# Performance work log

Measured on AMD Instinct MI355X. Metric: run time of the kernel, lower is better.

The kernel has to match this reference:

```python
import jax, jax.numpy as jnp
import numpy as np

B, C, Hf, Wf, HM, P = 64, 2048, 16, 16, 256, 10  # P = num_parts, NP = graph nodes
NP = P - 1
EPS = 1e-5  # BatchNorm eps

def bn_eval(x, g, b, rm, rv):
    return (x - rm) * jax.lax.rsqrt(rv + EPS) * g + b

def setup_inputs() -> dict:
    key = jax.random.key(0)
    ks = jax.random.split(key, 6)
    return {
        "x_global": jax.random.normal(ks[0], (B, C, Hf, Wf), jnp.float32),
        "x_gcn": jax.random.normal(ks[1], (B, C, Hf, Wf), jnp.float32),
        "mask": jax.random.randint(ks[2], (B, 1, HM, HM), 0, P, jnp.int32),
        "adj": jax.random.uniform(ks[3], (B, NP, NP), jnp.float32),
        "W1": jax.random.normal(ks[4], (C, C), jnp.float32) * 0.02,
        "b1": jnp.zeros((C,), jnp.float32),
        "g1": jnp.ones((NP * C,), jnp.float32), "be1": jnp.zeros((NP * C,), jnp.float32),
        "rm1": jnp.zeros((NP * C,), jnp.float32), "rv1": jnp.ones((NP * C,), jnp.float32),
        "W2": jax.random.normal(ks[5], (C, C), jnp.float32) * 0.02,
        "b2": jnp.zeros((C,), jnp.float32),
        "g2": jnp.ones((NP * C,), jnp.float32), "be2": jnp.zeros((NP * C,), jnp.float32),
        "rm2": jnp.zeros((NP * C,), jnp.float32), "rv2": jnp.ones((NP * C,), jnp.float32),
        "gb_g": jnp.ones((C,), jnp.float32), "gb_b": jnp.zeros((C,), jnp.float32),
        "gb_rm": jnp.zeros((C,), jnp.float32), "gb_rv": jnp.ones((C,), jnp.float32),
        "gn_g": jnp.ones((C,), jnp.float32), "gn_b": jnp.zeros((C,), jnp.float32),
        "gn_rm": jnp.zeros((C,), jnp.float32), "gn_rv": jnp.ones((C,), jnp.float32),
    }

def gc_layer(x, adj, Wt, bias, g, be, rm, rv):
    # GraphConvolution: matmul -> bmm(adj) -> bias -> BN over flattened (B, NP*C)
    s = jnp.einsum('bpc,cd->bpd', x, Wt)
    o = jnp.einsum('bpq,bqd->bpd', adj, s) + bias
    flat = o.reshape(o.shape[0], -1)
    return bn_eval(flat, g, be, rm, rv).reshape(o.shape)

def reference(x_global, x_gcn, mask, adj, W1, b1, g1, be1, rm1, rv1,
              W2, b2, g2, be2, rm2, rv2, gb_g, gb_b, gb_rm, gb_rv,
              gn_g, gn_b, gn_rm, gn_rv):
    # --- global branch: GAP + bottleneck BN (eval) ---
    feat_global = x_global.mean(axis=(2, 3))                      # (B, C)
    bnfeat_global = bn_eval(feat_global, gb_g, gb_b, gb_rm, gb_rv)

    # --- nearest-neighbor downsample of mask to feature-map size ---
    stride = HM // Hf
    mr = mask[:, 0, ::stride, ::stride]                           # (B, h, w)

    # one-hot part masks for classes 1..P-1: (B, h, w, NP)
    onehot = (mr[..., None] == jnp.arange(1, P)).astype(jnp.float32)
    counts = onehot.sum(axis=(1, 2))                              # (B, NP)

    # deterministic part dropout: drop the first present part per image
    drop = jnp.argmax(counts > 0, axis=1) + 1                     # (B,)
    keep = (mr != drop[:, None, None]).astype(jnp.float32)        # (B, h, w)
    x_self = x_gcn * keep[:, None, :, :]

    # segment mean pooling per part: (B, NP, C)
    denom = (counts + 1e-8)[..., None]
    mask_feat = jnp.einsum('bchw,bhwp->bpc', x_gcn, onehot) / denom
    self_feat = jnp.einsum('bchw,bhwp->bpc', x_self, onehot) / denom

    def gcn(x):
        x1 = jax.nn.relu(gc_layer(x, adj, W1, b1, g1, be1, rm1, rv1))
        x2 = jax.nn.relu(gc_layer(x1, adj, W2, b2, g2, be2, rm2, rv2))
        return x2.mean(axis=1), x2.reshape(x2.shape[0], -1)

    feat_gcn, feat_gcn_cat = gcn(mask_feat)
    feat_self, feat_self_cat = gcn(self_feat)
    bnfeat_gcn = bn_eval(feat_gcn, gn_g, gn_b, gn_rm, gn_rv)
    bnfeat_self = bn_eval(feat_self, gn_g, gn_b, gn_rm, gn_rv)

    # concatenate eval-mode outputs into one array: (B, 3*C + 2*NP*C)
    return jnp.concatenate([bnfeat_global, bnfeat_gcn, bnfeat_self,
                            feat_gcn_cat, feat_self_cat], axis=1)
```

## Files before the change

kernel.cpp:

```cpp
#include <hip/hip_runtime.h>
#include <cstdint>
#include <cstddef>

#define EPSV 1e-5f
#define GK 2048

typedef __bf16 bf16x8 __attribute__((ext_vector_type(8)));
typedef float f32x4 __attribute__((ext_vector_type(4)));

__device__ __forceinline__ unsigned short f2bf(float f) {
  unsigned int u = __float_as_uint(f);
  u += 0x7FFFu + ((u >> 16) & 1u);
  return (unsigned short)(u >> 16);
}

__device__ __forceinline__ void async_copy16(const void* src, void* dst_lds) {
  __builtin_amdgcn_global_load_lds(
      (const __attribute__((address_space(1))) void*)src,
      (__attribute__((address_space(3))) void*)dst_lds, 16, 0, 0);
}

__global__ __launch_bounds__(256) void ingest(
    const float* __restrict__ x, const int* __restrict__ mask,
    unsigned short* __restrict__ Abuf,
    const float* __restrict__ W1, const float* __restrict__ W2,
    unsigned short* __restrict__ Wt1, unsigned short* __restrict__ Wt2,
    const float* __restrict__ xg, const float* __restrict__ gb_g,
    const float* __restrict__ gb_b, const float* __restrict__ gb_rm,
    const float* __restrict__ gb_rv, float* __restrict__ out,
    const float* __restrict__ b1, const float* __restrict__ g1,
    const float* __restrict__ be1, const float* __restrict__ rm1,
    const float* __restrict__ rv1, const float* __restrict__ b2,
    const float* __restrict__ g2, const float* __restrict__ be2,
    const float* __restrict__ rm2, const float* __restrict__ rv2,
    float* __restrict__ sc1, float* __restrict__ sh1,
    float* __restrict__ sc2, float* __restrict__ sh2) {
  __shared__ union {
    struct {
      unsigned short As[64 * 264];
      unsigned short Bs[16 * 264];
      int pid[256];
      int cnt[10];
      float inv[9];
      int dm1;
    } pool;
    float tile[32][33];
  } sm;

  const int blk = blockIdx.x;
  const int t = threadIdx.x;

  if (blk < 2048) {
    const int b = blk >> 5;
    const int c0 = (blk & 31) * 64;

    int m = mask[(size_t)b * 65536 + (t >> 4) * 4096 + (t & 15) * 16];
    if (t < 10) sm.pool.cnt[t] = 0;
    __syncthreads();
    atomicAdd(&sm.pool.cnt[m], 1);
    sm.pool.pid[t] = m;

    const float4* xgp = (const float4*)(x + ((size_t)(b * 2048 + c0)) * 256);
#pragma unroll
    for (int it = 0; it < 16; it++) {
      int idx = t + it * 256;
      float4 v = xgp[idx];
      int row = idx >> 6, sc = (idx & 63) * 4;
      ushort4 h;
      h.x = f2bf(v.x); h.y = f2bf(v.y); h.z = f2bf(v.z); h.w = f2bf(v.w);
      *(ushort4*)&sm.pool.As[row * 264 + sc] = h;
    }
    __syncthreads();

    {
      int p = t >> 4, s0 = (t & 15) * 16;
#pragma unroll
      for (int j = 0; j < 16; j++)
        sm.pool.Bs[p * 264 + s0 + j] = (sm.pool.pid[s0 + j] == p + 1)
                                           ? (unsigned short)0x3F80
                                           : (unsigned short)0;
    }
    if (t == 0) {
      int dp = 0;
      for (int p = 8; p >= 0; p--)
        if (sm.pool.cnt[p + 1] > 0) dp = p;
      sm.pool.dm1 = dp;
    }
    if (t < 9) sm.pool.inv[t] = 1.f / ((float)sm.pool.cnt[t + 1] + 1e-8f);
    __syncthreads();

    const int wave = t >> 6;
    const int l16 = t & 15;
    const int quad = (t & 63) >> 4;
    f32x4 acc = (f32x4){0.f, 0.f, 0.f, 0.f};
#pragma unroll
    for (int ks = 0; ks < 8; ks++) {
      bf16x8 a =
          *(const bf16x8*)&sm.pool.As[(wave * 16 + l16) * 264 + ks * 32 + quad * 8];
      bf16x8 bf =
          *(const bf16x8*)&sm.pool.Bs[l16 * 264 + ks * 32 + quad * 8];
      acc = __builtin_amdgcn_mfma_f32_16x16x32_bf16(a, bf, acc, 0, 0, 0);
    }

    if (l16 < 9) {
      int p = l16;
      float inv = sm.pool.inv[p];
      int dm1 = sm.pool.dm1;
      int cbase = c0 + wave * 16 + quad * 4;
      ushort4 hm;
      hm.x = f2bf(acc[0] * inv);
      hm.y = f2bf(acc[1] * inv);
      hm.z = f2bf(acc[2] * inv);
      hm.w = f2bf(acc[3] * inv);
      ushort4 hs = (p == dm1) ? (ushort4){0, 0, 0, 0} : hm;
      *(ushort4*)&Abuf[(size_t)(b * 9 + p) * 2048 + cbase] = hm;
      *(ushort4*)&Abuf[(size_t)((64 + b) * 9 + p) * 2048 + cbase] = hs;
    }
  } else if (blk < 10240) {
    int rem = blk - 2048;
    int z = rem >> 12;
    rem &= 4095;
    int by = rem >> 6, bx = rem & 63;
    const float* W = z ? W2 : W1;
    unsigned short* Wt = z ? Wt2 : Wt1;
    int tx = t & 31;
    int ty = t >> 5;
    int k0 = by * 32, n0 = bx * 32;
#pragma unroll
    for (int i = 0; i < 32; i += 8)
      sm.tile[ty + i][tx] = W[(size_t)(k0 + ty + i) * 2048 + n0 + tx];
    __syncthreads();
#pragma unroll
    for (int i = 0; i < 32; i += 8)
      Wt[(size_t)(n0 + ty + i) * 2048 + k0 + tx] = f2bf(sm.tile[tx][ty + i]);
  } else if (blk < 18432) {
    int base = (blk - 10240) * 16 + (t >> 6) * 4;
    int lane = t & 63;
    const float4* xp = (const float4*)xg + (size_t)base * 64 + lane;
    float4 v0 = xp[0], v1 = xp[64], v2 = xp[128], v3 = xp[192];
    float s0 = v0.x + v0.y + v0.z + v0.w;
    float s1 = v1.x + v1.y + v1.z + v1.w;
    float s2 = v2.x + v2.y + v2.z + v2.w;
    float s3 = v3.x + v3.y + v3.z + v3.w;
#pragma unroll
    for (int o = 32; o > 0; o >>= 1) {
      s0 += __shfl_xor(s0, o, 64);
      s1 += __shfl_xor(s1, o, 64);
      s2 += __shfl_xor(s2, o, 64);
      s3 += __shfl_xor(s3, o, 64);
    }
    if (lane == 0) {
      int b = base >> 11, c = base & 2047;
      float mm[4] = {s0 * (1.f / 256.f), s1 * (1.f / 256.f),
                     s2 * (1.f / 256.f), s3 * (1.f / 256.f)};
      float4 o4;
      float* po = &o4.x;
#pragma unroll
      for (int r = 0; r < 4; r++) {
        int cc = c + r;
        po[r] = (mm[r] - gb_rm[cc]) / sqrtf(gb_rv[cc] + EPSV) * gb_g[cc] +
                gb_b[cc];
      }
      *(float4*)(out + (size_t)b * 43008 + c) = o4;
    }
  } else {
    int i = (blk - 18432) * 256 + t;
    int z = i >= 18432;
    int f = i - z * 18432;
    int d = f & 2047;
    const float* g = z ? g2 : g1;
    const float* be = z ? be2 : be1;
    const float* rm = z ? rm2 : rm1;
    const float* rv = z ? rv2 : rv1;
    const float* bias = z ? b2 : b1;
    float sc = g[f] / sqrtf(rv[f] + EPSV);
    float sh = (bias[d] - rm[f]) * sc + be[f];
    (z ? sc2 : sc1)[f] = sc;
    (z ? sh2 : sh1)[f] = sh;
  }
}

#define SPART (1152 * 2048)
__global__ __launch_bounds__(256) void gemm_db(
    const unsigned short* __restrict__ A, const unsigned short* __restrict__ Bt,
    float* __restrict__ S) {
  __shared__ unsigned short As[2][128 * 64];
  __shared__ unsigned short Bs[2][64 * 64];
  const int tid = threadIdx.x;
  const int lane = tid & 63;
  const int wave = tid >> 6;
  const int wm = (wave >> 1) << 6;
  const int wn = (wave & 1) << 5;
  const int quad = lane >> 4;
  const int l16 = lane & 15;
  const int by = blockIdx.y;
  const int bx = blockIdx.x;
  const int kz = blockIdx.z;

  const unsigned short* Ag = A + (size_t)by * 128 * GK;
  const unsigned short* Bg = Bt + (size_t)bx * 64 * GK;
  S += (size_t)kz * SPART;

  f32x4 acc[4][2];
#pragma unroll
  for (int i = 0; i < 4; i++)
#pragma unroll
    for (int j = 0; j < 2; j++) acc[i][j] = (f32x4){0.f, 0.f, 0.f, 0.f};

  int srA[4], scA[4];
#pragma unroll
  for (int s = 0; s < 4; s++) {
    int idx = tid + s * 256;
    srA[s] = idx >> 3;
    scA[s] = ((idx & 7) ^ (srA[s] & 7)) * 8;
  }
  int srB[2], scB[2];
#pragma unroll
  for (int s = 0; s < 2; s++) {
    int idx = tid + s * 256;
    srB[s] = idx >> 3;
    scB[s] = ((idx & 7) ^ (srB[s] & 7)) * 8;
  }

  const int kbeg = kz * 1024;

#define STAGE(buf, kk)                                                        \
  do {                                                                        \
    _Pragma("unroll") for (int s = 0; s < 4; s++) {                           \
      int idx = tid + s * 256;                                                \
      async_copy16(Ag + (size_t)srA[s] * GK + (kk) + scA[s],                  \
                   &As[buf][idx * 8]);                                        \
    }                                                                         \
    _Pragma("unroll") for (int s = 0; s < 2; s++) {                           \
      int idx = tid + s * 256;                                                \
      async_copy16(Bg + (size_t)srB[s] * GK + (kk) + scB[s],                  \
                   &Bs[buf][idx * 8]);                                        \
    }                                                                         \
  } while (0)

  STAGE(0, kbeg);
  asm volatile("s_waitcnt vmcnt(0)" ::: "memory");
  __syncthreads();

  for (int it = 0; it < 16; it++) {
    const int cur = it & 1;
    if (it < 15) STAGE(cur ^ 1, kbeg + (it + 1) * 64);

#pragma unroll
    for (int ks = 0; ks < 2; ks++) {
      bf16x8 af[4], bfr[2];
#pragma unroll
      for (int i = 0; i < 4; i++) {
        int row = wm + i * 16 + l16;
        int slot = row * 8 + ((ks * 4 + quad) ^ (row & 7));
        af[i] = *(const bf16x8*)&As[cur][slot * 8];
      }
#pragma unroll
      for (int j = 0; j < 2; j++) {
        int row = wn + j * 16 + l16;
        int slot = row * 8 + ((ks * 4 + quad) ^ (row & 7));
        bfr[j] = *(const bf16x8*)&Bs[cur][slot * 8];
      }
#pragma unroll
      for (int i = 0; i < 4; i++)
#pragma unroll
        for (int j = 0; j < 2; j++)
          acc[i][j] = __builtin_amdgcn_mfma_f32_16x16x32_bf16(
              af[i], bfr[j], acc[i][j], 0, 0, 0);
    }

    if (it < 15) {
      asm volatile("s_waitcnt vmcnt(0)" ::: "memory");
      __syncthreads();
    }
  }
#undef STAGE

#pragma unroll
  for (int i = 0; i < 4; i++)
#pragma unroll
    for (int j = 0; j < 2; j++)
#pragma unroll
      for (int r = 0; r < 4; r++) {
        int m = by * 128 + wm + i * 16 + quad * 4 + r;
        int n = bx * 64 + wn + j * 16 + l16;
        S[(size_t)m * 2048 + n] = acc[i][j][r];
      }
}

__global__ __launch_bounds__(256) void epi_mid(
    const float* __restrict__ S, const float* __restrict__ adj,
    const float* __restrict__ sc, const float* __restrict__ sh,
    unsigned short* __restrict__ Aout) {
  int idx = blockIdx.x * 256 + threadIdx.x;
  int d = idx & 2047;
  int bb = idx >> 11;
  int b = bb & 63;
  float s[9];
#pragma unroll
  for (int q = 0; q < 9; q++) {
    size_t off = (size_t)(bb * 9 + q) * 2048 + d;
    s[q] = S[off] + S[off + SPART];
  }
#pragma unroll
  for (int p = 0; p < 9; p++) {
    float o = 0.f;
#pragma unroll
    for (int q = 0; q < 9; q++) o += adj[b * 81 + p * 9 + q] * s[q];
    int f = p * 2048 + d;
    float v = fmaxf(o * sc[f] + sh[f], 0.f);
    Aout[(size_t)(bb * 9 + p) * 2048 + d] = f2bf(v);
  }
}

__global__ __launch_bounds__(256) void epi_final(
    const float* __restrict__ S, const float* __restrict__ adj,
    const float* __restrict__ sc, const float* __restrict__ sh,
    const float* __restrict__ gn_g, const float* __restrict__ gn_b,
    const float* __restrict__ gn_rm, const float* __restrict__ gn_rv,
    float* __restrict__ out) {
  int idx = blockIdx.x * 256 + threadIdx.x;
  int d = idx & 2047;
  int bb = idx >> 11;
  int b = bb & 63;
  bool selfb = bb >= 64;
  float s[9];
#pragma unroll
  for (int q = 0; q < 9; q++) {
    size_t off = (size_t)(bb * 9 + q) * 2048 + d;
    s[q] = S[off] + S[off + SPART];
  }
  float* orow = out + (size_t)b * 43008;
  size_t catbase = selfb ? 24576 : 6144;
  float mean = 0.f;
#pragma unroll
  for (int p = 0; p < 9; p++) {
    float o = 0.f;
#pragma unroll
    for (int q = 0; q < 9; q++) o += adj[b * 81 + p * 9 + q] * s[q];
    int f = p * 2048 + d;
    float v = fmaxf(o * sc[f] + sh[f], 0.f);
    mean += v;
    orow[catbase + f] = v;
  }
  mean *= (1.f / 9.f);
  orow[(selfb ? 4096 : 2048) + d] =
      (mean - gn_rm[d]) / sqrtf(gn_rv[d] + EPSV) * gn_g[d] + gn_b[d];
}

extern "C" void kernel_launch(void* const* d_in, const int* in_sizes, int n_in,
                              void* d_out, int out_size, void* d_ws,
                              size_t ws_size, hipStream_t stream) {
  const float* x_global = (const float*)d_in[0];
  const float* x_gcn = (const float*)d_in[1];
  const int* mask = (const int*)d_in[2];
  const float* adj = (const float*)d_in[3];
  const float* W1 = (const float*)d_in[4];
  const float* b1 = (const float*)d_in[5];
  const float* g1 = (const float*)d_in[6];
  const float* be1 = (const float*)d_in[7];
  const float* rm1 = (const float*)d_in[8];
  const float* rv1 = (const float*)d_in[9];
  const float* W2 = (const float*)d_in[10];
  const float* b2 = (const float*)d_in[11];
  const float* g2 = (const float*)d_in[12];
  const float* be2 = (const float*)d_in[13];
  const float* rm2 = (const float*)d_in[14];
  const float* rv2 = (const float*)d_in[15];
  const float* gb_g = (const float*)d_in[16];
  const float* gb_b = (const float*)d_in[17];
  const float* gb_rm = (const float*)d_in[18];
  const float* gb_rv = (const float*)d_in[19];
  const float* gn_g = (const float*)d_in[20];
  const float* gn_b = (const float*)d_in[21];
  const float* gn_rm = (const float*)d_in[22];
  const float* gn_rv = (const float*)d_in[23];
  float* out = (float*)d_out;

  char* ws = (char*)d_ws;
  unsigned short* Abuf = (unsigned short*)(ws);
  unsigned short* Wt1 = (unsigned short*)(ws + 4718592);
  unsigned short* Wt2 = (unsigned short*)(ws + 13107200);
  float* S = (float*)(ws + 21495808);
  float* sc1 = (float*)(ws + 40370176);
  float* sh1 = (float*)(ws + 40443904);
  float* sc2 = (float*)(ws + 40517632);
  float* sh2 = (float*)(ws + 40591360);

  ingest<<<18576, 256, 0, stream>>>(x_gcn, mask, Abuf, W1, W2, Wt1, Wt2,
                                    x_global, gb_g, gb_b, gb_rm, gb_rv, out,
                                    b1, g1, be1, rm1, rv1, b2, g2, be2, rm2,
                                    rv2, sc1, sh1, sc2, sh2);
  gemm_db<<<dim3(32, 9, 2), 256, 0, stream>>>(Abuf, Wt1, S);
  epi_mid<<<1024, 256, 0, stream>>>(S, adj, sc1, sh1, Abuf);
  gemm_db<<<dim3(32, 9, 2), 256, 0, stream>>>(Abuf, Wt2, S);
  epi_final<<<1024, 256, 0, stream>>>(S, adj, sc2, sh2, gn_g, gn_b, gn_rm,
                                      gn_rv, out);
}
```

Before: 406.2 us.

## Split pooling into its own kernel loading MFMA operands directly from global

```diff
diff --git a/kernel.cpp b/kernel.cpp
--- a/kernel.cpp
+++ b/kernel.cpp
@@ -20,9 +20,71 @@
       (__attribute__((address_space(3))) void*)dst_lds, 16, 0, 0);
 }
 
-__global__ __launch_bounds__(256) void ingest(
+__global__ __launch_bounds__(256) void pool(
     const float* __restrict__ x, const int* __restrict__ mask,
-    unsigned short* __restrict__ Abuf,
+    unsigned short* __restrict__ Abuf) {
+  __shared__ unsigned char pid8[256];
+  __shared__ int cnt[10];
+  const int t = threadIdx.x;
+  const int b = blockIdx.x >> 5;
+  const int c0 = (blockIdx.x & 31) * 64;
+
+  int m = mask[(size_t)b * 65536 + (t >> 4) * 4096 + (t & 15) * 16];
+  if (t < 10) cnt[t] = 0;
+  __syncthreads();
+  atomicAdd(&cnt[m], 1);
+  pid8[t] = (unsigned char)m;
+  __syncthreads();
+
+  const int w = t >> 6;
+  const int l16 = t & 15;
+  const int quad = (t & 63) >> 4;
+  const float* xrow = x + ((size_t)(b * 2048 + c0 + w * 16 + l16)) * 256;
+  const unsigned int tgt = (unsigned int)(l16 + 1);
+
+  f32x4 acc = (f32x4){0.f, 0.f, 0.f, 0.f};
+#pragma unroll
+  for (int ks = 0; ks < 8; ks++) {
+    const float4 va = *(const float4*)(xrow + ks * 32 + quad * 8);
+    const float4 vb = *(const float4*)(xrow + ks * 32 + quad * 8 + 4);
+    uint2 pc = *(const uint2*)&pid8[ks * 32 + quad * 8];
+    union { bf16x8 v; unsigned int u[4]; } bfr;
+#pragma unroll
+    for (int d = 0; d < 4; d++) {
+      unsigned int word = (d < 2) ? pc.x : pc.y;
+      unsigned int sh = (d & 1) * 16;
+      unsigned int b0 = (word >> sh) & 0xFFu;
+      unsigned int b1 = (word >> (sh + 8)) & 0xFFu;
+      bfr.u[d] = (b0 == tgt ? 0x3F80u : 0u) | (b1 == tgt ? 0x3F800000u : 0u);
+    }
+    bf16x8 af;
+    af[0] = (__bf16)va.x; af[1] = (__bf16)va.y;
+    af[2] = (__bf16)va.z; af[3] = (__bf16)va.w;
+    af[4] = (__bf16)vb.x; af[5] = (__bf16)vb.y;
+    af[6] = (__bf16)vb.z; af[7] = (__bf16)vb.w;
+    acc = __builtin_amdgcn_mfma_f32_16x16x32_bf16(af, bfr.v, acc, 0, 0, 0);
+  }
+
+  if (l16 < 9) {
+    const int p = l16;
+    float invp = 1.f / ((float)cnt[p + 1] + 1e-8f);
+    int dm1 = 0;
+#pragma unroll
+    for (int q = 8; q >= 0; q--)
+      if (cnt[q + 1] > 0) dm1 = q;
+    int cbase = c0 + w * 16 + quad * 4;
+    ushort4 hm;
+    hm.x = f2bf(acc[0] * invp);
+    hm.y = f2bf(acc[1] * invp);
+    hm.z = f2bf(acc[2] * invp);
+    hm.w = f2bf(acc[3] * invp);
+    ushort4 hs = (p == dm1) ? (ushort4){0, 0, 0, 0} : hm;
+    *(ushort4*)&Abuf[(size_t)(b * 9 + p) * 2048 + cbase] = hm;
+    *(ushort4*)&Abuf[(size_t)((64 + b) * 9 + p) * 2048 + cbase] = hs;
+  }
+}
+
+__global__ __launch_bounds__(256) void prep(
     const float* __restrict__ W1, const float* __restrict__ W2,
     unsigned short* __restrict__ Wt1, unsigned short* __restrict__ Wt2,
     const float* __restrict__ xg, const float* __restrict__ gb_g,
@@ -35,91 +97,13 @@
     const float* __restrict__ rm2, const float* __restrict__ rv2,
     float* __restrict__ sc1, float* __restrict__ sh1,
     float* __restrict__ sc2, float* __restrict__ sh2) {
-  __shared__ union {
-    struct {
-      unsigned short As[64 * 264];
-      unsigned short Bs[16 * 264];
-      int pid[256];
-      int cnt[10];
-      float inv[9];
-      int dm1;
-    } pool;
-    float tile[32][33];
-  } sm;
-
+  __shared__ float tile[32][33];
   const int blk = blockIdx.x;
   const int t = threadIdx.x;
 
-  if (blk < 2048) {
-    const int b = blk >> 5;
-    const int c0 = (blk & 31) * 64;
-
-    int m = mask[(size_t)b * 65536 + (t >> 4) * 4096 + (t & 15) * 16];
-    if (t < 10) sm.pool.cnt[t] = 0;
-    __syncthreads();
-    atomicAdd(&sm.pool.cnt[m], 1);
-    sm.pool.pid[t] = m;
-
-    const float4* xgp = (const float4*)(x + ((size_t)(b * 2048 + c0)) * 256);
-#pragma unroll
-    for (int it = 0; it < 16; it++) {
-      int idx = t + it * 256;
-      float4 v = xgp[idx];
-      int row = idx >> 6, sc = (idx & 63) * 4;
-      ushort4 h;
-      h.x = f2bf(v.x); h.y = f2bf(v.y); h.z = f2bf(v.z); h.w = f2bf(v.w);
-      *(ushort4*)&sm.pool.As[row * 264 + sc] = h;
-    }
-    __syncthreads();
-
-    {
-      int p = t >> 4, s0 = (t & 15) * 16;
-#pragma unroll
-      for (int j = 0; j < 16; j++)
-        sm.pool.Bs[p * 264 + s0 + j] = (sm.pool.pid[s0 + j] == p + 1)
-                                           ? (unsigned short)0x3F80
-                                           : (unsigned short)0;
-    }
-    if (t == 0) {
-      int dp = 0;
-      for (int p = 8; p >= 0; p--)
-        if (sm.pool.cnt[p + 1] > 0) dp = p;
-      sm.pool.dm1 = dp;
-    }
-    if (t < 9) sm.pool.inv[t] = 1.f / ((float)sm.pool.cnt[t + 1] + 1e-8f);
-    __syncthreads();
-
-    const int wave = t >> 6;
-    const int l16 = t & 15;
-    const int quad = (t & 63) >> 4;
-    f32x4 acc = (f32x4){0.f, 0.f, 0.f, 0.f};
-#pragma unroll
-    for (int ks = 0; ks < 8; ks++) {
-      bf16x8 a =
-          *(const bf16x8*)&sm.pool.As[(wave * 16 + l16) * 264 + ks * 32 + quad * 8];
-      bf16x8 bf =
-          *(const bf16x8*)&sm.pool.Bs[l16 * 264 + ks * 32 + quad * 8];
-      acc = __builtin_amdgcn_mfma_f32_16x16x32_bf16(a, bf, acc, 0, 0, 0);
-    }
-
-    if (l16 < 9) {
-      int p = l16;
-      float inv = sm.pool.inv[p];
-      int dm1 = sm.pool.dm1;
-      int cbase = c0 + wave * 16 + quad * 4;
-      ushort4 hm;
-      hm.x = f2bf(acc[0] * inv);
-      hm.y = f2bf(acc[1] * inv);
-      hm.z = f2bf(acc[2] * inv);
-      hm.w = f2bf(acc[3] * inv);
-      ushort4 hs = (p == dm1) ? (ushort4){0, 0, 0, 0} : hm;
-      *(ushort4*)&Abuf[(size_t)(b * 9 + p) * 2048 + cbase] = hm;
-      *(ushort4*)&Abuf[(size_t)((64 + b) * 9 + p) * 2048 + cbase] = hs;
-    }
-  } else if (blk < 10240) {
-    int rem = blk - 2048;
-    int z = rem >> 12;
-    rem &= 4095;
+  if (blk < 8192) {
+    int z = blk >> 12;
+    int rem = blk & 4095;
     int by = rem >> 6, bx = rem & 63;
     const float* W = z ? W2 : W1;
     unsigned short* Wt = z ? Wt2 : Wt1;
@@ -128,13 +112,13 @@
     int k0 = by * 32, n0 = bx * 32;
 #pragma unroll
     for (int i = 0; i < 32; i += 8)
-      sm.tile[ty + i][tx] = W[(size_t)(k0 + ty + i) * 2048 + n0 + tx];
+      tile[ty + i][tx] = W[(size_t)(k0 + ty + i) * 2048 + n0 + tx];
     __syncthreads();
 #pragma unroll
     for (int i = 0; i < 32; i += 8)
-      Wt[(size_t)(n0 + ty + i) * 2048 + k0 + tx] = f2bf(sm.tile[tx][ty + i]);
-  } else if (blk < 18432) {
-    int base = (blk - 10240) * 16 + (t >> 6) * 4;
+      Wt[(size_t)(n0 + ty + i) * 2048 + k0 + tx] = f2bf(tile[tx][ty + i]);
+  } else if (blk < 16384) {
+    int base = (blk - 8192) * 16 + (t >> 6) * 4;
     int lane = t & 63;
     const float4* xp = (const float4*)xg + (size_t)base * 64 + lane;
     float4 v0 = xp[0], v1 = xp[64], v2 = xp[128], v3 = xp[192];
@@ -164,7 +148,7 @@
       *(float4*)(out + (size_t)b * 43008 + c) = o4;
     }
   } else {
-    int i = (blk - 18432) * 256 + t;
+    int i = (blk - 16384) * 256 + t;
     int z = i >= 18432;
     int f = i - z * 18432;
     int d = f & 2047;
@@ -387,10 +371,10 @@
   float* sc2 = (float*)(ws + 40517632);
   float* sh2 = (float*)(ws + 40591360);
 
-  ingest<<<18576, 256, 0, stream>>>(x_gcn, mask, Abuf, W1, W2, Wt1, Wt2,
-                                    x_global, gb_g, gb_b, gb_rm, gb_rv, out,
-                                    b1, g1, be1, rm1, rv1, b2, g2, be2, rm2,
-                                    rv2, sc1, sh1, sc2, sh2);
+  pool<<<2048, 256, 0, stream>>>(x_gcn, mask, Abuf);
+  prep<<<16528, 256, 0, stream>>>(W1, W2, Wt1, Wt2, x_global, gb_g, gb_b,
+                                  gb_rm, gb_rv, out, b1, g1, be1, rm1, rv1,
+                                  b2, g2, be2, rm2, rv2, sc1, sh1, sc2, sh2);
   gemm_db<<<dim3(32, 9, 2), 256, 0, stream>>>(Abuf, Wt1, S);
   epi_mid<<<1024, 256, 0, stream>>>(S, adj, sc1, sh1, Abuf);
   gemm_db<<<dim3(32, 9, 2), 256, 0, stream>>>(Abuf, Wt2, S);
```

After: 410.2 us. No clear change (+1.0%).

## Derive self-branch first GCN layer from full branch by linearity

Applied to the files above, without the earlier changes.

```diff
diff --git a/kernel.cpp b/kernel.cpp
--- a/kernel.cpp
+++ b/kernel.cpp
@@ -22,7 +22,7 @@
 
 __global__ __launch_bounds__(256) void ingest(
     const float* __restrict__ x, const int* __restrict__ mask,
-    unsigned short* __restrict__ Abuf,
+    unsigned short* __restrict__ Abuf, int* __restrict__ dropm1,
     const float* __restrict__ W1, const float* __restrict__ W2,
     unsigned short* __restrict__ Wt1, unsigned short* __restrict__ Wt2,
     const float* __restrict__ xg, const float* __restrict__ gb_g,
@@ -42,7 +42,6 @@
       int pid[256];
       int cnt[10];
       float inv[9];
-      int dm1;
     } pool;
     float tile[32][33];
   } sm;
@@ -80,11 +79,11 @@
                                            ? (unsigned short)0x3F80
                                            : (unsigned short)0;
     }
-    if (t == 0) {
+    if (t == 0 && (blk & 31) == 0) {
       int dp = 0;
       for (int p = 8; p >= 0; p--)
         if (sm.pool.cnt[p + 1] > 0) dp = p;
-      sm.pool.dm1 = dp;
+      dropm1[b] = dp;
     }
     if (t < 9) sm.pool.inv[t] = 1.f / ((float)sm.pool.cnt[t + 1] + 1e-8f);
     __syncthreads();
@@ -105,16 +104,13 @@
     if (l16 < 9) {
       int p = l16;
       float inv = sm.pool.inv[p];
-      int dm1 = sm.pool.dm1;
       int cbase = c0 + wave * 16 + quad * 4;
       ushort4 hm;
       hm.x = f2bf(acc[0] * inv);
       hm.y = f2bf(acc[1] * inv);
       hm.z = f2bf(acc[2] * inv);
       hm.w = f2bf(acc[3] * inv);
-      ushort4 hs = (p == dm1) ? (ushort4){0, 0, 0, 0} : hm;
       *(ushort4*)&Abuf[(size_t)(b * 9 + p) * 2048 + cbase] = hm;
-      *(ushort4*)&Abuf[(size_t)((64 + b) * 9 + p) * 2048 + cbase] = hs;
     }
   } else if (blk < 10240) {
     int rem = blk - 2048;
@@ -183,7 +179,7 @@
 #define SPART (1152 * 2048)
 __global__ __launch_bounds__(256) void gemm_db(
     const unsigned short* __restrict__ A, const unsigned short* __restrict__ Bt,
-    float* __restrict__ S) {
+    float* __restrict__ S, int mlimit) {
   __shared__ unsigned short As[2][128 * 64];
   __shared__ unsigned short Bs[2][64 * 64];
   const int tid = threadIdx.x;
@@ -284,32 +280,36 @@
       for (int r = 0; r < 4; r++) {
         int m = by * 128 + wm + i * 16 + quad * 4 + r;
         int n = bx * 64 + wn + j * 16 + l16;
-        S[(size_t)m * 2048 + n] = acc[i][j][r];
+        if (m < mlimit) S[(size_t)m * 2048 + n] = acc[i][j][r];
       }
 }
 
 __global__ __launch_bounds__(256) void epi_mid(
     const float* __restrict__ S, const float* __restrict__ adj,
-    const float* __restrict__ sc, const float* __restrict__ sh,
-    unsigned short* __restrict__ Aout) {
+    const int* __restrict__ dropm1, const float* __restrict__ sc,
+    const float* __restrict__ sh, unsigned short* __restrict__ Aout) {
   int idx = blockIdx.x * 256 + threadIdx.x;
   int d = idx & 2047;
-  int bb = idx >> 11;
-  int b = bb & 63;
+  int b = idx >> 11;
   float s[9];
 #pragma unroll
   for (int q = 0; q < 9; q++) {
-    size_t off = (size_t)(bb * 9 + q) * 2048 + d;
+    size_t off = (size_t)(b * 9 + q) * 2048 + d;
     s[q] = S[off] + S[off + SPART];
   }
+  int dm1 = dropm1[b];
+  float sd = s[dm1];
 #pragma unroll
   for (int p = 0; p < 9; p++) {
     float o = 0.f;
 #pragma unroll
     for (int q = 0; q < 9; q++) o += adj[b * 81 + p * 9 + q] * s[q];
+    float os = o - adj[b * 81 + p * 9 + dm1] * sd;
     int f = p * 2048 + d;
-    float v = fmaxf(o * sc[f] + sh[f], 0.f);
-    Aout[(size_t)(bb * 9 + p) * 2048 + d] = f2bf(v);
+    float scv = sc[f], shv = sh[f];
+    Aout[(size_t)(b * 9 + p) * 2048 + d] = f2bf(fmaxf(o * scv + shv, 0.f));
+    Aout[(size_t)((64 + b) * 9 + p) * 2048 + d] =
+        f2bf(fmaxf(os * scv + shv, 0.f));
   }
 }
 
@@ -386,14 +386,15 @@
   float* sh1 = (float*)(ws + 40443904);
   float* sc2 = (float*)(ws + 40517632);
   float* sh2 = (float*)(ws + 40591360);
-
-  ingest<<<18576, 256, 0, stream>>>(x_gcn, mask, Abuf, W1, W2, Wt1, Wt2,
-                                    x_global, gb_g, gb_b, gb_rm, gb_rv, out,
-                                    b1, g1, be1, rm1, rv1, b2, g2, be2, rm2,
-                                    rv2, sc1, sh1, sc2, sh2);
-  gemm_db<<<dim3(32, 9, 2), 256, 0, stream>>>(Abuf, Wt1, S);
-  epi_mid<<<1024, 256, 0, stream>>>(S, adj, sc1, sh1, Abuf);
-  gemm_db<<<dim3(32, 9, 2), 256, 0, stream>>>(Abuf, Wt2, S);
+  int* dropm1 = (int*)(ws + 40665088);
+
+  ingest<<<18576, 256, 0, stream>>>(x_gcn, mask, Abuf, dropm1, W1, W2, Wt1,
+                                    Wt2, x_global, gb_g, gb_b, gb_rm, gb_rv,
+                                    out, b1, g1, be1, rm1, rv1, b2, g2, be2,
+                                    rm2, rv2, sc1, sh1, sc2, sh2);
+  gemm_db<<<dim3(32, 5, 2), 256, 0, stream>>>(Abuf, Wt1, S, 576);
+  epi_mid<<<512, 256, 0, stream>>>(S, adj, dropm1, sc1, sh1, Abuf);
+  gemm_db<<<dim3(32, 9, 2), 256, 0, stream>>>(Abuf, Wt2, S, 1152);
   epi_final<<<1024, 256, 0, stream>>>(S, adj, sc2, sh2, gn_g, gn_b, gn_rm,
                                       gn_rv, out);
 }
```

New measurement: 405.6 us. No clear change (-0.1%).
